# Performance work log

Hardware: AMD Instinct MI355X
Metric: run time of the kernel (lower is better)

## Reference

```python
import jax, jax.numpy as jnp
import numpy as np
import math

# Model dims (from VisionMamba defaults)
D = 768        # embed_dim
DI = 1536      # d_inner = 2*D
N = 16         # d_state
R = 48         # dt_rank = ceil(D/16)
K = 4          # d_conv
DEPTH = 24
B = 4
H, W, P, CIN = 1280, 960, 64, 3
GH, GW = H // P, W // P
NPATCH = GH * GW           # 300
L = NPATCH + 1             # 301 with cls token
POS = NPATCH // 2          # middle cls token position = 150
NCLS = 1000
EPS = 1e-5


def setup_inputs() -> dict:
    key = jax.random.key(0)
    c = [0]
    def nk():
        c[0] += 1
        return jax.random.fold_in(key, c[0])
    def rn(shape, s=0.02):
        return jax.random.normal(nk(), shape, jnp.float32) * s
    inp = {}
    inp['img'] = jax.random.normal(nk(), (B, CIN, H, W), jnp.float32)
    inp['patch_w'] = rn((D, CIN, P, P))
    inp['patch_b'] = jnp.zeros((D,), jnp.float32)
    inp['cls_token'] = rn((1, 1, D))
    inp['pos_embed'] = rn((1, L, D))
    inp['norm_w'] = jnp.ones((DEPTH, D), jnp.float32)
    inp['in_proj_w'] = rn((DEPTH, 2 * DI, D))
    for s in ('f', 'b'):
        inp[f'conv_{s}_w'] = rn((DEPTH, DI, K), 0.1)
        inp[f'conv_{s}_b'] = jnp.zeros((DEPTH, DI), jnp.float32)
        inp[f'xproj_{s}_w'] = rn((DEPTH, R + 2 * N, DI))
        inp[f'dt_{s}_w'] = rn((DEPTH, DI, R), 0.1)
        dtv = jnp.exp(jax.random.uniform(nk(), (DEPTH, DI), jnp.float32,
                                         math.log(1e-3), math.log(1e-1)))
        inp[f'dt_{s}_b'] = jnp.log(jnp.expm1(dtv))  # softplus-inverse init
        inp[f'A_{s}_log'] = jnp.broadcast_to(
            jnp.log(jnp.arange(1, N + 1, dtype=jnp.float32)), (DEPTH, DI, N)) + 0.0
        inp[f'D_{s}'] = jnp.ones((DEPTH, DI), jnp.float32)
    inp['out_proj_w'] = rn((DEPTH, D, DI))
    inp['norm_f_w'] = jnp.ones((D,), jnp.float32)
    inp['head_w'] = rn((NCLS, D))
    inp['head_b'] = jnp.zeros((NCLS,), jnp.float32)
    return inp


def _rms(x, w):
    return x * jax.lax.rsqrt(jnp.mean(x * x, axis=-1, keepdims=True) + EPS) * w


def _silu(x):
    return x * jax.nn.sigmoid(x)


def _cconv(x, w, b):
    # depthwise causal conv1d, x: [B,L,DI], w: [DI,K]
    Lx = x.shape[1]
    xp = jnp.pad(x, ((0, 0), (K - 1, 0), (0, 0)))
    return sum(xp[:, k:k + Lx, :] * w[:, k] for k in range(K)) + b


def _ssm(xc, z, xproj_w, dt_w, dt_b, A_log, Dp):
    # selective scan; xc, z: [B,L,DI]
    dbl = jnp.einsum('bld,ed->ble', xc, xproj_w)        # [B,L,R+2N]
    dt_r, Bm, Cm = dbl[..., :R], dbl[..., R:R + N], dbl[..., R + N:]
    dt = jax.nn.softplus(jnp.einsum('blr,dr->bld', dt_r, dt_w) + dt_b)
    A = -jnp.exp(A_log)                                 # [DI,N]
    dA = jnp.exp(dt[..., None] * A)                     # [B,L,DI,N]
    dBu = (dt * xc)[..., None] * Bm[:, :, None, :]      # [B,L,DI,N]
    def step(h, ab):
        a, bu = ab
        h = a * h + bu
        return h, h
    h0 = jnp.zeros((dA.shape[0], DI, N), dA.dtype)
    _, hs = jax.lax.scan(step, h0, (jnp.swapaxes(dA, 0, 1), jnp.swapaxes(dBu, 0, 1)))
    y = jnp.einsum('lbdn,bln->bld', hs, Cm) + xc * Dp
    return y * _silu(z)


def _mixer(h, p):
    (in_w, cfw, cfb, xfw, dtfw, dtfb, Afl, Df,
     cbw, cbb, xbw, dtbw, dtbb, Abl, Db, ow) = p
    xz = jnp.einsum('bld,ed->ble', h, in_w)
    x, z = xz[..., :DI], xz[..., DI:]
    yf = _ssm(_silu(_cconv(x, cfw, cfb)), z, xfw, dtfw, dtfb, Afl, Df)
    xr, zr = x[:, ::-1], z[:, ::-1]
    yb = _ssm(_silu(_cconv(xr, cbw, cbb)), zr, xbw, dtbw, dtbb, Abl, Db)
    y = (yf + yb[:, ::-1]) * 0.5   # bimamba v2 with if_divide_out=True
    return jnp.einsum('ble,de->bld', y, ow)


def _forward(img, patch_w, patch_b, cls_token, pos_embed, norm_w, in_proj_w,
             conv_f_w, conv_f_b, xproj_f_w, dt_f_w, dt_f_b, A_f_log, D_f,
             conv_b_w, conv_b_b, xproj_b_w, dt_b_w, dt_b_b, A_b_log, D_b,
             out_proj_w, norm_f_w, head_w, head_b):
    Bn = img.shape[0]
    # non-overlapping conv patch embed (kernel == stride == 64)
    x = img.reshape(Bn, CIN, GH, P, GW, P)
    x = jnp.einsum('bcipjq,dcpq->bijd', x, patch_w).reshape(Bn, NPATCH, D) + patch_b
    cls = jnp.broadcast_to(cls_token, (Bn, 1, D))
    x = jnp.concatenate([x[:, :POS], cls, x[:, POS:]], axis=1) + pos_embed
    layer_params = (norm_w, in_proj_w, conv_f_w, conv_f_b, xproj_f_w, dt_f_w,
                    dt_f_b, A_f_log, D_f, conv_b_w, conv_b_b, xproj_b_w,
                    dt_b_w, dt_b_b, A_b_log, D_b, out_proj_w)
    def layer(carry, p):
        h, res = carry
        res = res + h                # fused add-norm: Add -> RMSNorm -> Mixer
        hn = _rms(res, p[0])
        h2 = _mixer(hn, p[1:])
        return (h2, res), None
    (h, res), _ = jax.lax.scan(layer, (x, jnp.zeros_like(x)), layer_params)
    out = _rms(res + h, norm_f_w)
    return jnp.einsum('bd,cd->bc', out[:, POS], head_w) + head_b


def reference(img, patch_w, patch_b, cls_token, pos_embed, norm_w, in_proj_w,
              conv_f_w, conv_f_b, xproj_f_w, dt_f_w, dt_f_b, A_f_log, D_f,
              conv_b_w, conv_b_b, xproj_b_w, dt_b_w, dt_b_b, A_b_log, D_b,
              out_proj_w, norm_f_w, head_w, head_b):
    return _forward(img, patch_w, patch_b, cls_token, pos_embed, norm_w,
                    in_proj_w, conv_f_w, conv_f_b, xproj_f_w, dt_f_w, dt_f_b,
                    A_f_log, D_f, conv_b_w, conv_b_b, xproj_b_w, dt_b_w,
                    dt_b_b, A_b_log, D_b, out_proj_w, norm_f_w, head_w, head_b)
```

## Files before the change

kernel.cpp:

```cpp
#include <hip/hip_runtime.h>
#include <hip/hip_bf16.h>
#include <math.h>

#define B_ 4
#define L_ 301
#define D_ 768
#define DI_ 1536
#define NP_ 300
#define POS_ 150
#define M_ 1204
#define NC_ 5
#define CL_ 64

typedef __bf16 bf16;
typedef __attribute__((ext_vector_type(8))) __bf16 bf16x8;
typedef __attribute__((ext_vector_type(4))) float floatx4;

__device__ __forceinline__ float siluf(float x) { return x / (1.f + __expf(-x)); }
__device__ __forceinline__ float softplusf(float x) { return x > 20.f ? x : log1pf(__expf(x)); }

__global__ __launch_bounds__(256) void gemm_mfma(
    const bf16* __restrict__ A0, const bf16* __restrict__ A1, int lda,
    const float* __restrict__ W0, const float* __restrict__ W1, int ldw,
    const float* __restrict__ bias0, const float* __restrict__ bias1,
    float* __restrict__ C0, float* __restrict__ C1,
    bf16* __restrict__ Cb0, bf16* __restrict__ Cb1, int ldc,
    int M, int Nw, int Kw, int Ksteps, int act)
{
    const int zz = blockIdx.z;
    const bf16* A = zz ? A1 : A0;
    const float* W = zz ? W1 : W0;
    const float* bias = zz ? bias1 : bias0;
    float* C = zz ? C1 : C0;
    bf16* Cb = zz ? Cb1 : Cb0;

    __shared__ bf16 As[128 * 32];
    __shared__ bf16 Ws[128 * 32];
    const int t = threadIdx.x;
    const int bm = blockIdx.y * 128;
    const int bn = blockIdx.x * 128;
    const int lane = t & 63;
    const int wid = t >> 6;
    const int wr = wid >> 1, wc = wid & 1;
    const int ar = t >> 2;
    const int ac = (t & 3) * 8;

    const bool fullNK = ((Nw & 127) == 0) && ((Kw & 31) == 0);

    floatx4 acc[4][4] = {};

    for (int ks = 0; ks < Ksteps; ks++) {
        const int k0 = ks * 32;
#pragma unroll
        for (int c2 = 0; c2 < 2; c2++) {
            int r = ar + c2 * 64;
            int gm = bm + r; if (gm >= M) gm = M - 1;
            const bf16* gp = A + (size_t)gm * lda + k0 + ac;
            __builtin_amdgcn_global_load_lds(
                (const __attribute__((address_space(1))) void*)gp,
                (__attribute__((address_space(3))) void*)(As + r * 32 + ac),
                16, 0, 0);
        }
#pragma unroll
        for (int c2 = 0; c2 < 2; c2++) {
            int r = ar + c2 * 64;
            int gn = bn + r;
            float vv[8];
            if (fullNK) {
                const floatx4* wp4 = (const floatx4*)(W + (size_t)gn * ldw + k0 + ac);
                floatx4 a4 = wp4[0], b4 = wp4[1];
#pragma unroll
                for (int e = 0; e < 4; e++) { vv[e] = a4[e]; vv[e + 4] = b4[e]; }
            } else {
                const float* wp = W + (size_t)gn * ldw + k0 + ac;
#pragma unroll
                for (int e = 0; e < 8; e++) {
                    int kk = k0 + ac + e;
                    vv[e] = (gn < Nw && kk < Kw) ? wp[e] : 0.f;
                }
            }
            bf16x8 pk;
#pragma unroll
            for (int e = 0; e < 8; e++) pk[e] = (bf16)vv[e];
            *(bf16x8*)(Ws + r * 32 + ac) = pk;
        }
        __syncthreads();
        const int ra = wr * 64 + (lane & 15);
        const int rb = wc * 64 + (lane & 15);
        const int kb = (lane >> 4) * 8;
        bf16x8 af[4], bfm[4];
#pragma unroll
        for (int i = 0; i < 4; i++)
            af[i] = *(const bf16x8*)(As + (ra + i * 16) * 32 + kb);
#pragma unroll
        for (int j = 0; j < 4; j++)
            bfm[j] = *(const bf16x8*)(Ws + (rb + j * 16) * 32 + kb);
#pragma unroll
        for (int i = 0; i < 4; i++)
#pragma unroll
            for (int j = 0; j < 4; j++)
                acc[i][j] = __builtin_amdgcn_mfma_f32_16x16x32_bf16(af[i], bfm[j], acc[i][j], 0, 0, 0);
        __syncthreads();
    }
#pragma unroll
    for (int i = 0; i < 4; i++) {
#pragma unroll
        for (int j = 0; j < 4; j++) {
            int n = bn + wc * 64 + j * 16 + (lane & 15);
            if (n >= Nw) continue;
            float bv = (act >= 1) ? bias[n] : 0.f;
#pragma unroll
            for (int r = 0; r < 4; r++) {
                int m = bm + wr * 64 + i * 16 + (lane >> 4) * 4 + r;
                if (m >= M) continue;
                float v = acc[i][j][r] + bv;
                if (act == 2) v = softplusf(v);
                C[(size_t)m * ldc + n] = v;
                if (Cb) Cb[(size_t)m * ldc + n] = (bf16)v;
            }
        }
    }
}

__global__ __launch_bounds__(256) void gemm_mfma_sk(
    const bf16* __restrict__ A0, const bf16* __restrict__ A1, int lda,
    const float* __restrict__ W0, const float* __restrict__ W1, int ldw,
    float* __restrict__ Cp, size_t chunkStride, int ldc,
    int M, int Nw, int KstepsPer, int SK)
{
    const int z = blockIdx.z;
    const int dir = z / SK;
    const int chunk = z % SK;
    const bf16* A = dir ? A1 : A0;
    const float* W = dir ? W1 : W0;
    float* C = Cp + (size_t)z * chunkStride;

    __shared__ bf16 As[128 * 32];
    __shared__ bf16 Ws[128 * 32];
    const int t = threadIdx.x;
    const int bm = blockIdx.y * 128;
    const int bn = blockIdx.x * 128;
    const int lane = t & 63;
    const int wid = t >> 6;
    const int wr = wid >> 1, wc = wid & 1;
    const int ar = t >> 2;
    const int ac = (t & 3) * 8;

    floatx4 acc[4][4] = {};

    for (int ks = 0; ks < KstepsPer; ks++) {
        const int k0 = (chunk * KstepsPer + ks) * 32;
#pragma unroll
        for (int c2 = 0; c2 < 2; c2++) {
            int r = ar + c2 * 64;
            int gm = bm + r; if (gm >= M) gm = M - 1;
            const bf16* gp = A + (size_t)gm * lda + k0 + ac;
            __builtin_amdgcn_global_load_lds(
                (const __attribute__((address_space(1))) void*)gp,
                (__attribute__((address_space(3))) void*)(As + r * 32 + ac),
                16, 0, 0);
        }
#pragma unroll
        for (int c2 = 0; c2 < 2; c2++) {
            int r = ar + c2 * 64;
            int gn = bn + r;
            bf16x8 pk;
            if (gn < Nw) {
                const floatx4* wp4 = (const floatx4*)(W + (size_t)gn * ldw + k0 + ac);
                floatx4 a4 = wp4[0], b4 = wp4[1];
#pragma unroll
                for (int e = 0; e < 4; e++) { pk[e] = (bf16)a4[e]; pk[e + 4] = (bf16)b4[e]; }
            } else {
#pragma unroll
                for (int e = 0; e < 8; e++) pk[e] = (bf16)0.f;
            }
            *(bf16x8*)(Ws + r * 32 + ac) = pk;
        }
        __syncthreads();
        const int ra = wr * 64 + (lane & 15);
        const int rb = wc * 64 + (lane & 15);
        const int kb = (lane >> 4) * 8;
        bf16x8 af[4], bfm[4];
#pragma unroll
        for (int i = 0; i < 4; i++)
            af[i] = *(const bf16x8*)(As + (ra + i * 16) * 32 + kb);
#pragma unroll
        for (int j = 0; j < 4; j++)
            bfm[j] = *(const bf16x8*)(Ws + (rb + j * 16) * 32 + kb);
#pragma unroll
        for (int i = 0; i < 4; i++)
#pragma unroll
            for (int j = 0; j < 4; j++)
                acc[i][j] = __builtin_amdgcn_mfma_f32_16x16x32_bf16(af[i], bfm[j], acc[i][j], 0, 0, 0);
        __syncthreads();
    }
#pragma unroll
    for (int i = 0; i < 4; i++) {
#pragma unroll
        for (int j = 0; j < 4; j++) {
            int n = bn + wc * 64 + j * 16 + (lane & 15);
            if (n >= Nw) continue;
#pragma unroll
            for (int r = 0; r < 4; r++) {
                int m = bm + wr * 64 + i * 16 + (lane >> 4) * 4 + r;
                if (m >= M) continue;
                C[(size_t)m * ldc + n] = acc[i][j][r];
            }
        }
    }
}

__global__ __launch_bounds__(256) void gemm_mfma_avg_sk(
    const bf16* __restrict__ Af, const bf16* __restrict__ Ab, int lda,
    const float* __restrict__ W, int ldw,
    float* __restrict__ Cp, size_t chunkStride, int ldc,
    int M, int Nw, int KstepsPer, int SK)
{
    const int chunk = blockIdx.z;
    float* C = Cp + (size_t)chunk * chunkStride;

    __shared__ bf16 As[128 * 32];
    __shared__ bf16 Ws[128 * 32];
    const int t = threadIdx.x;
    const int bm = blockIdx.y * 128;
    const int bn = blockIdx.x * 128;
    const int lane = t & 63;
    const int wid = t >> 6;
    const int wr = wid >> 1, wc = wid & 1;
    const int ar = t >> 2;
    const int ac = (t & 3) * 8;

    floatx4 acc[4][4] = {};

    for (int ks = 0; ks < KstepsPer; ks++) {
        const int k0 = (chunk * KstepsPer + ks) * 32;
#pragma unroll
        for (int c2 = 0; c2 < 2; c2++) {
            int r = ar + c2 * 64;
            int gm = bm + r; if (gm >= M) gm = M - 1;
            bf16x8 a8 = *(const bf16x8*)(Af + (size_t)gm * lda + k0 + ac);
            bf16x8 b8 = *(const bf16x8*)(Ab + (size_t)gm * lda + k0 + ac);
            bf16x8 pk;
#pragma unroll
            for (int e = 0; e < 8; e++)
                pk[e] = (bf16)(0.5f * ((float)a8[e] + (float)b8[e]));
            *(bf16x8*)(As + r * 32 + ac) = pk;
        }
#pragma unroll
        for (int c2 = 0; c2 < 2; c2++) {
            int r = ar + c2 * 64;
            int gn = bn + r;
            const floatx4* wp4 = (const floatx4*)(W + (size_t)gn * ldw + k0 + ac);
            floatx4 a4 = wp4[0], b4 = wp4[1];
            bf16x8 pk;
#pragma unroll
            for (int e = 0; e < 4; e++) { pk[e] = (bf16)a4[e]; pk[e + 4] = (bf16)b4[e]; }
            *(bf16x8*)(Ws + r * 32 + ac) = pk;
        }
        __syncthreads();
        const int ra = wr * 64 + (lane & 15);
        const int rb = wc * 64 + (lane & 15);
        const int kb = (lane >> 4) * 8;
        bf16x8 af[4], bfm[4];
#pragma unroll
        for (int i = 0; i < 4; i++)
            af[i] = *(const bf16x8*)(As + (ra + i * 16) * 32 + kb);
#pragma unroll
        for (int j = 0; j < 4; j++)
            bfm[j] = *(const bf16x8*)(Ws + (rb + j * 16) * 32 + kb);
#pragma unroll
        for (int i = 0; i < 4; i++)
#pragma unroll
            for (int j = 0; j < 4; j++)
                acc[i][j] = __builtin_amdgcn_mfma_f32_16x16x32_bf16(af[i], bfm[j], acc[i][j], 0, 0, 0);
        __syncthreads();
    }
#pragma unroll
    for (int i = 0; i < 4; i++) {
#pragma unroll
        for (int j = 0; j < 4; j++) {
            int n = bn + wc * 64 + j * 16 + (lane & 15);
            if (n >= Nw) continue;
#pragma unroll
            for (int r = 0; r < 4; r++) {
                int m = bm + wr * 64 + i * 16 + (lane >> 4) * 4 + r;
                if (m >= M) continue;
                C[(size_t)m * ldc + n] = acc[i][j][r];
            }
        }
    }
}

__global__ void reduce_sk2(const float* __restrict__ Cp, size_t chunkStride, int SK,
                           const float* __restrict__ bias0,
                           float* __restrict__ C0, float* __restrict__ C1,
                           bf16* __restrict__ Cb0, bf16* __restrict__ Cb1,
                           int total, int ldn, int act)
{
    const int dir = blockIdx.y;
    const float* P = Cp + (size_t)dir * SK * chunkStride;
    float* C = dir ? C1 : C0;
    bf16* Cb = dir ? Cb1 : Cb0;
    int idx = blockIdx.x * 256 + threadIdx.x;
    if (idx >= total) return;
    float s = 0.f;
    for (int c = 0; c < SK; c++) s += P[(size_t)c * chunkStride + idx];
    if (act >= 1) s += bias0[idx % ldn];
    if (act == 2) s = softplusf(s);
    C[idx] = s;
    if (Cb) Cb[idx] = (bf16)s;
}

__global__ __launch_bounds__(256) void gemm_patch_mfma(
    const float* __restrict__ img, const float* __restrict__ W,
    float* __restrict__ Cp)
{
    __shared__ bf16 As[128 * 32];
    __shared__ bf16 Ws[128 * 32];
    const int t = threadIdx.x;
    const int bm = blockIdx.y * 128;
    const int bn = blockIdx.x * 128;
    const int chunk = blockIdx.z;
    const int lane = t & 63;
    const int wid = t >> 6;
    const int wr = wid >> 1, wc = wid & 1;
    const int ar = t >> 2;
    const int ac = (t & 3) * 8;
    const int M = 1200, ldw = 12288, ldc = 768;
    float* C = Cp + (size_t)chunk * M * ldc;

    const float* abase[2];
#pragma unroll
    for (int c2 = 0; c2 < 2; c2++) {
        int gm = bm + ar + c2 * 64; if (gm >= M) gm = M - 1;
        int b = gm / 300, rem = gm % 300;
        int gi = rem / 15, gj = rem % 15;
        abase[c2] = img + ((size_t)(b * 3) * 1280 + gi * 64) * 960 + gj * 64;
    }

    floatx4 acc[4][4] = {};

    for (int ks = 0; ks < 48; ks++) {
        const int k0 = (chunk * 48 + ks) * 32;
        const int k = k0 + ac;
        const int q = k & 63, p = (k >> 6) & 63, c = k >> 12;
#pragma unroll
        for (int c2 = 0; c2 < 2; c2++) {
            int r = ar + c2 * 64;
            const float* ip = abase[c2] + ((size_t)c * 1280 + p) * 960 + q;
            const floatx4* ip4 = (const floatx4*)ip;
            floatx4 a4 = ip4[0], b4 = ip4[1];
            bf16x8 pk;
#pragma unroll
            for (int e = 0; e < 4; e++) { pk[e] = (bf16)a4[e]; pk[e + 4] = (bf16)b4[e]; }
            *(bf16x8*)(As + r * 32 + ac) = pk;
        }
#pragma unroll
        for (int c2 = 0; c2 < 2; c2++) {
            int r = ar + c2 * 64;
            int gn = bn + r;
            const floatx4* wp4 = (const floatx4*)(W + (size_t)gn * ldw + k);
            floatx4 a4 = wp4[0], b4 = wp4[1];
            bf16x8 pk;
#pragma unroll
            for (int e = 0; e < 4; e++) { pk[e] = (bf16)a4[e]; pk[e + 4] = (bf16)b4[e]; }
            *(bf16x8*)(Ws + r * 32 + ac) = pk;
        }
        __syncthreads();
        const int ra = wr * 64 + (lane & 15);
        const int rb = wc * 64 + (lane & 15);
        const int kb = (lane >> 4) * 8;
        bf16x8 af[4], bfm[4];
#pragma unroll
        for (int i = 0; i < 4; i++)
            af[i] = *(const bf16x8*)(As + (ra + i * 16) * 32 + kb);
#pragma unroll
        for (int j = 0; j < 4; j++)
            bfm[j] = *(const bf16x8*)(Ws + (rb + j * 16) * 32 + kb);
#pragma unroll
        for (int i = 0; i < 4; i++)
#pragma unroll
            for (int j = 0; j < 4; j++)
                acc[i][j] = __builtin_amdgcn_mfma_f32_16x16x32_bf16(af[i], bfm[j], acc[i][j], 0, 0, 0);
        __syncthreads();
    }
#pragma unroll
    for (int i = 0; i < 4; i++) {
#pragma unroll
        for (int j = 0; j < 4; j++) {
            int n = bn + wc * 64 + j * 16 + (lane & 15);
#pragma unroll
            for (int r = 0; r < 4; r++) {
                int m = bm + wr * 64 + i * 16 + (lane >> 4) * 4 + r;
                if (m >= M) continue;
                C[(size_t)m * ldc + n] = acc[i][j][r];
            }
        }
    }
}

__global__ void gemm_bt(const float* __restrict__ A, int lda,
                        const float* __restrict__ W, int ldw,
                        const float* __restrict__ bias,
                        float* __restrict__ C, int ldc,
                        int M, int N, int K, int act) {
    __shared__ float As[16][68];
// ... 116 lines not shown
    const float* bias = rev ? bb_ : bf_;
    float* out = rev ? ob : of;
    bf16* outb = rev ? obb : ofb;
    int d = idx % DI_;
    int l = (idx / DI_) % L_;
    int b = idx / (DI_ * L_);
    float acc = bias[d];
#pragma unroll
    for (int k = 0; k < 4; k++) {
        int ls = l - 3 + k;
        if (ls < 0) continue;
        int lsrc = rev ? (L_ - 1 - ls) : ls;
        acc += xz[((long)(b * L_ + lsrc)) * (2 * DI_) + d] * w[d * 4 + k];
    }
    float v = siluf(acc);
    out[idx] = v;
    outb[idx] = (bf16)v;
}

__global__ __launch_bounds__(256) void ssm_p1(
    const float* __restrict__ xcF, const float* __restrict__ dtF, const float* __restrict__ dblF,
    const float* __restrict__ xcB, const float* __restrict__ dtB, const float* __restrict__ dblB,
    const float* __restrict__ AF, const float* __restrict__ AB,
    float* __restrict__ Hend, float* __restrict__ Aprod)
{
    const int rev = blockIdx.y;
    const int c = blockIdx.z;
    const float* xc = rev ? xcB : xcF;
    const float* dt = rev ? dtB : dtF;
    const float* dbl = rev ? dblB : dblF;
    const float* Alog = rev ? AB : AF;

    const int t = threadIdx.x;
    const int n = t & 15;
    const int g = t >> 4;
    const int gb = blockIdx.x;
    const int b = gb / (DI_ / 16);
    const int d0 = (gb % (DI_ / 16)) * 16;
    const int d = d0 + g;

    __shared__ float dt_s[CL_][16];
    __shared__ float xc_s[CL_][16];
    __shared__ float bm_s[CL_][16];

    const float a = -__expf(Alog[(size_t)d * 16 + n]);
    const size_t rowbase = (size_t)b * L_;
    const int c0 = c * CL_;

    for (int i = t; i < CL_ * 16; i += 256) {
        int ll = i >> 4, dd = i & 15;
        int l = c0 + ll;
        size_t r = (rowbase + l) * DI_ + d0 + dd;
        dt_s[ll][dd] = dt[r];
        xc_s[ll][dd] = xc[r];
        bm_s[ll][dd] = dbl[(rowbase + l) * 80 + 48 + dd];
    }
    __syncthreads();

    float h = 0.f, sdt = 0.f;
#pragma unroll 4
    for (int ll = 0; ll < CL_; ll++) {
        float dtv = dt_s[ll][g];
        float xcv = xc_s[ll][g];
        float bm = bm_s[ll][n];
        h = __expf(dtv * a) * h + dtv * xcv * bm;
        sdt += dtv;
    }
    size_t o = (((size_t)rev * (NC_ - 1) + c) * 384 + gb) * 256 + t;
    Hend[o] = h;
    Aprod[o] = __expf(a * sdt);
}

__global__ __launch_bounds__(256) void ssm_p2(
    const float* __restrict__ xcF, const float* __restrict__ dtF, const float* __restrict__ dblF,
    const float* __restrict__ xcB, const float* __restrict__ dtB, const float* __restrict__ dblB,
    const float* __restrict__ xz,
    const float* __restrict__ AF, const float* __restrict__ DF,
    const float* __restrict__ AB, const float* __restrict__ DB,
    const float* __restrict__ Hend, const float* __restrict__ Aprod,
    bf16* __restrict__ yF, bf16* __restrict__ yB)
{
    const int rev = blockIdx.y;
    const int c = blockIdx.z;
    const float* xc = rev ? xcB : xcF;
    const float* dt = rev ? dtB : dtF;
    const float* dbl = rev ? dblB : dblF;
    const float* Alog = rev ? AB : AF;
    const float* Dp = rev ? DB : DF;
    bf16* yout = rev ? yB : yF;

    const int t = threadIdx.x;
    const int n = t & 15;
    const int g = t >> 4;
    const int gb = blockIdx.x;
    const int b = gb / (DI_ / 16);
    const int d0 = (gb % (DI_ / 16)) * 16;
    const int d = d0 + g;

    __shared__ float dt_s[CL_][16];
    __shared__ float xc_s[CL_][16];
    __shared__ float z_s[CL_][16];
    __shared__ float bm_s[CL_][16];
    __shared__ float cm_s[CL_][16];
    __shared__ float y_s[CL_][16];

    const float a = -__expf(Alog[(size_t)d * 16 + n]);
    const float Dv = Dp[d];
    const size_t rowbase = (size_t)b * L_;
    const int c0 = c * CL_;
    const int Tc = min(CL_, L_ - c0);

    for (int i = t; i < Tc * 16; i += 256) {
        int ll = i >> 4, dd = i & 15;
        int l = c0 + ll;
        size_t r = (rowbase + l) * DI_ + d0 + dd;
        dt_s[ll][dd] = dt[r];
        xc_s[ll][dd] = xc[r];
        int lz = rev ? (L_ - 1 - l) : l;
        z_s[ll][dd] = xz[(rowbase + lz) * (2 * DI_) + DI_ + d0 + dd];
        bm_s[ll][dd] = dbl[(rowbase + l) * 80 + 48 + dd];
        cm_s[ll][dd] = dbl[(rowbase + l) * 80 + 64 + dd];
    }

    float h = 0.f;
    for (int j = 0; j < c; j++) {
        size_t o = (((size_t)rev * (NC_ - 1) + j) * 384 + gb) * 256 + t;
        h = Aprod[o] * h + Hend[o];
    }
    __syncthreads();

#pragma unroll 4
    for (int ll = 0; ll < Tc; ll++) {
        float dtv = dt_s[ll][g];
        float xcv = xc_s[ll][g];
        float bm = bm_s[ll][n];
        float cm = cm_s[ll][n];
        h = __expf(dtv * a) * h + dtv * xcv * bm;
        float cc = h * cm;
        cc += __shfl_xor(cc, 1);
        cc += __shfl_xor(cc, 2);
        cc += __shfl_xor(cc, 4);
        cc += __shfl_xor(cc, 8);
        if (n == 0) {
            float yv = (cc + xcv * Dv) * siluf(z_s[ll][g]);
            y_s[ll][g] = yv;
        }
    }
    __syncthreads();

    for (int i = t; i < Tc * 16; i += 256) {
        int ll = i >> 4, dd = i & 15;
        int l = c0 + ll;
        int lo = rev ? (L_ - 1 - l) : l;
        yout[(rowbase + lo) * DI_ + d0 + dd] = (bf16)y_s[ll][dd];
    }
}

__global__ void final_rms(const float* __restrict__ res, const float* __restrict__ h,
                          const float* __restrict__ w, float* __restrict__ out) {
    int b = blockIdx.x;
    long base = ((long)b * L_ + POS_) * D_;
    float v[3];
    float ss = 0.f;
#pragma unroll
    for (int i = 0; i < 3; i++) {
        int d = threadIdx.x + i * 256;
        float t = res[base + d] + h[base + d];
        v[i] = t;
        ss += t * t;
    }
#pragma unroll
    for (int off = 1; off < 64; off <<= 1) ss += __shfl_xor(ss, off);
    __shared__ float red[4];
    __shared__ float inv;
    if ((threadIdx.x & 63) == 0) red[threadIdx.x >> 6] = ss;
    __syncthreads();
    if (threadIdx.x == 0) {
// ... 37 lines not shown
    const float* norm_f_w = (const float*)d_in[22];
    const float* head_w = (const float*)d_in[23];
    const float* head_b = (const float*)d_in[24];

    char* p8 = (char*)d_ws;
    auto alloc = [&](size_t nb) { char* r = p8; p8 += (nb + 255) & ~(size_t)255; return r; };
    float* x    = (float*)alloc((size_t)M_ * D_ * 4);
    float* res  = (float*)alloc((size_t)M_ * D_ * 4);
    bf16*  hnb  = (bf16*) alloc((size_t)M_ * D_ * 2);
    float* xz   = (float*)alloc((size_t)M_ * 2 * DI_ * 4);
    float* xcf  = (float*)alloc((size_t)M_ * DI_ * 4);
    float* xcb  = (float*)alloc((size_t)M_ * DI_ * 4);
    bf16*  xcfb = (bf16*) alloc((size_t)M_ * DI_ * 2);
    bf16*  xcbb = (bf16*) alloc((size_t)M_ * DI_ * 2);
    float* dtf  = (float*)alloc((size_t)M_ * DI_ * 4);
    float* dtb  = (float*)alloc((size_t)M_ * DI_ * 4);
    bf16*  yfb  = (bf16*) alloc((size_t)M_ * DI_ * 2);
    bf16*  ybb  = (bf16*) alloc((size_t)M_ * DI_ * 2);
    float* dblf = (float*)alloc((size_t)M_ * 80 * 4);
    float* dblb = (float*)alloc((size_t)M_ * 80 * 4);
    bf16*  dblfb= (bf16*) alloc((size_t)M_ * 80 * 2);
    bf16*  dblbb= (bf16*) alloc((size_t)M_ * 80 * 2);
    float* clsv = (float*)alloc((size_t)B_ * D_ * 4);
    float* hend = (float*)alloc((size_t)2 * (NC_ - 1) * 384 * 256 * 4);
    float* aprd = (float*)alloc((size_t)2 * (NC_ - 1) * 384 * 256 * 4);
    float* xtmp = dtf;

    float* patchP = xz;
    float* xprojP = dtf;
    float* outP   = dtf;

    gemm_patch_mfma<<<dim3(6, 10, 8), 256, 0, stream>>>(img, patch_w, patchP);
    reduce_sk2<<<dim3((1200 * 768 + 255) / 256, 1), 256, 0, stream>>>(
        patchP, (size_t)1200 * 768, 8, patch_b, xtmp, nullptr, nullptr, nullptr,
        1200 * 768, 768, 1);
    assemble<<<(B_ * L_ * D_ + 255) / 256, 256, 0, stream>>>(xtmp, cls_token, pos_embed, x, res);

    for (int layer = 0; layer < 24; layer++) {
        const float* ipw = in_proj_w + (size_t)layer * 2 * DI_ * D_;
        const float* cfw = conv_f_w + (size_t)layer * DI_ * 4;
        const float* cfb = conv_f_b + (size_t)layer * DI_;
        const float* xfw = xproj_f_w + (size_t)layer * 80 * DI_;
        const float* dfw = dt_f_w + (size_t)layer * DI_ * 48;
        const float* dfb = dt_f_b + (size_t)layer * DI_;
        const float* afl = A_f_log + (size_t)layer * DI_ * 16;
        const float* df = D_f + (size_t)layer * DI_;
        const float* cbw = conv_b_w + (size_t)layer * DI_ * 4;
        const float* cbb = conv_b_b + (size_t)layer * DI_;
        const float* xbw = xproj_b_w + (size_t)layer * 80 * DI_;
        const float* dbw = dt_b_w + (size_t)layer * DI_ * 48;
        const float* dbb = dt_b_b + (size_t)layer * DI_;
        const float* abl = A_b_log + (size_t)layer * DI_ * 16;
        const float* db = D_b + (size_t)layer * DI_;
        const float* opw = out_proj_w + (size_t)layer * D_ * DI_;
        const float* nw = norm_w + (size_t)layer * D_;

        add_rms<<<M_, 256, 0, stream>>>(res, x, nw, hnb);
        gemm_mfma<<<dim3(24, 10, 1), 256, 0, stream>>>(
            hnb, hnb, D_, ipw, ipw, D_, nullptr, nullptr,
            xz, xz, nullptr, nullptr, 2 * DI_, M_, 2 * DI_, D_, 24, 0);
        conv_silu2<<<dim3((B_ * L_ * DI_ + 255) / 256, 2), 256, 0, stream>>>(
            xz, cfw, cfb, cbw, cbb, xcf, xcfb, xcb, xcbb);
        gemm_mfma_sk<<<dim3(1, 10, 16), 256, 0, stream>>>(
            xcfb, xcbb, DI_, xfw, xbw, DI_,
            xprojP, (size_t)M_ * 80, 80, M_, 80, 6, 8);
        reduce_sk2<<<dim3((M_ * 80 + 255) / 256, 2), 256, 0, stream>>>(
            xprojP, (size_t)M_ * 80, 8, nullptr,
            dblf, dblb, dblfb, dblbb, M_ * 80, 80, 0);
        gemm_mfma<<<dim3(12, 10, 2), 256, 0, stream>>>(
            dblfb, dblbb, 80, dfw, dbw, 48, dfb, dbb,
            dtf, dtb, nullptr, nullptr, DI_, M_, DI_, 48, 2, 2);
        ssm_p1<<<dim3(384, 2, NC_ - 1), 256, 0, stream>>>(
            xcf, dtf, dblf, xcb, dtb, dblb, afl, abl, hend, aprd);
        ssm_p2<<<dim3(384, 2, NC_), 256, 0, stream>>>(
            xcf, dtf, dblf, xcb, dtb, dblb, xz, afl, df, abl, db,
            hend, aprd, yfb, ybb);
        gemm_mfma_avg_sk<<<dim3(6, 10, 4), 256, 0, stream>>>(
            yfb, ybb, DI_, opw, DI_,
            outP, (size_t)M_ * D_, D_, M_, D_, 12, 4);
        reduce_sk2<<<dim3((M_ * D_ + 255) / 256, 1), 256, 0, stream>>>(
            outP, (size_t)M_ * D_, 4, nullptr,
            x, nullptr, nullptr, nullptr, M_ * D_, D_, 0);
    }

    final_rms<<<B_, 256, 0, stream>>>(res, x, norm_f_w, clsv);
    gemm_bt<<<dim3(16, 1), 256, 0, stream>>>(clsv, D_, head_w, D_, head_b,
                                             (float*)d_out, 1000, B_, 1000, D_, 1);
}
```

Measured before the change: 6.487 ms.

## Double-buffer LDS tiles in all GEMMs and restructure SSM scan per channel

```diff
diff --git a/kernel.cpp b/kernel.cpp
--- a/kernel.cpp
+++ b/kernel.cpp
@@ -34,8 +34,8 @@
     float* C = zz ? C1 : C0;
     bf16* Cb = zz ? Cb1 : Cb0;
 
-    __shared__ bf16 As[128 * 32];
-    __shared__ bf16 Ws[128 * 32];
+    __shared__ bf16 As[2][128 * 32];
+    __shared__ bf16 Ws[2][128 * 32];
     const int t = threadIdx.x;
     const int bm = blockIdx.y * 128;
     const int bn = blockIdx.x * 128;
@@ -44,62 +44,106 @@
     const int wr = wid >> 1, wc = wid & 1;
     const int ar = t >> 2;
     const int ac = (t & 3) * 8;
-
     const bool fullNK = ((Nw & 127) == 0) && ((Kw & 31) == 0);
 
+    int gmr[2], gnr[2];
+#pragma unroll
+    for (int c2 = 0; c2 < 2; c2++) {
+        int gm = bm + ar + c2 * 64; if (gm >= M) gm = M - 1;
+        gmr[c2] = gm;
+        gnr[c2] = bn + ar + c2 * 64;
+    }
+
     floatx4 acc[4][4] = {};
+    float vv[2][8];
+
+#pragma unroll
+    for (int c2 = 0; c2 < 2; c2++) {
+        const bf16* gp = A + (size_t)gmr[c2] * lda + ac;
+        __builtin_amdgcn_global_load_lds(
+            (const __attribute__((address_space(1))) void*)gp,
+            (__attribute__((address_space(3))) void*)(&As[0][0] + (ar + c2 * 64) * 32 + ac),
+            16, 0, 0);
+    }
+#pragma unroll
+    for (int c2 = 0; c2 < 2; c2++) {
+        if (fullNK) {
+            const floatx4* wp4 = (const floatx4*)(W + (size_t)gnr[c2] * ldw + ac);
+            floatx4 a4 = wp4[0], b4 = wp4[1];
+#pragma unroll
+            for (int e = 0; e < 4; e++) { vv[c2][e] = a4[e]; vv[c2][e + 4] = b4[e]; }
+        } else {
+            const float* wp = W + (size_t)gnr[c2] * ldw + ac;
+#pragma unroll
+            for (int e = 0; e < 8; e++) {
+                int kk = ac + e;
+                vv[c2][e] = (gnr[c2] < Nw && kk < Kw) ? wp[e] : 0.f;
+            }
+        }
+    }
+#pragma unroll
+    for (int c2 = 0; c2 < 2; c2++) {
+        bf16x8 pk;
+#pragma unroll
+        for (int e = 0; e < 8; e++) pk[e] = (bf16)vv[c2][e];
+        *(bf16x8*)(&Ws[0][0] + (ar + c2 * 64) * 32 + ac) = pk;
+    }
+    __syncthreads();
 
     for (int ks = 0; ks < Ksteps; ks++) {
-        const int k0 = ks * 32;
-#pragma unroll
-        for (int c2 = 0; c2 < 2; c2++) {
-            int r = ar + c2 * 64;
-            int gm = bm + r; if (gm >= M) gm = M - 1;
-            const bf16* gp = A + (size_t)gm * lda + k0 + ac;
-            __builtin_amdgcn_global_load_lds(
-                (const __attribute__((address_space(1))) void*)gp,
-                (__attribute__((address_space(3))) void*)(As + r * 32 + ac),
-                16, 0, 0);
-        }
-#pragma unroll
-        for (int c2 = 0; c2 < 2; c2++) {
-            int r = ar + c2 * 64;
-            int gn = bn + r;
-            float vv[8];
-            if (fullNK) {
-                const floatx4* wp4 = (const floatx4*)(W + (size_t)gn * ldw + k0 + ac);
-                floatx4 a4 = wp4[0], b4 = wp4[1];
-#pragma unroll
-                for (int e = 0; e < 4; e++) { vv[e] = a4[e]; vv[e + 4] = b4[e]; }
-            } else {
-                const float* wp = W + (size_t)gn * ldw + k0 + ac;
-#pragma unroll
-                for (int e = 0; e < 8; e++) {
-                    int kk = k0 + ac + e;
-                    vv[e] = (gn < Nw && kk < Kw) ? wp[e] : 0.f;
+        const int cur = ks & 1, nxt = cur ^ 1;
+        const bool pf = (ks + 1 < Ksteps);
+        if (pf) {
+            const int k0 = (ks + 1) * 32;
+#pragma unroll
+            for (int c2 = 0; c2 < 2; c2++) {
+                const bf16* gp = A + (size_t)gmr[c2] * lda + k0 + ac;
+                __builtin_amdgcn_global_load_lds(
+                    (const __attribute__((address_space(1))) void*)gp,
+                    (__attribute__((address_space(3))) void*)(&As[nxt][0] + (ar + c2 * 64) * 32 + ac),
+                    16, 0, 0);
+            }
+#pragma unroll
+            for (int c2 = 0; c2 < 2; c2++) {
+                if (fullNK) {
+                    const floatx4* wp4 = (const floatx4*)(W + (size_t)gnr[c2] * ldw + k0 + ac);
+                    floatx4 a4 = wp4[0], b4 = wp4[1];
+#pragma unroll
+                    for (int e = 0; e < 4; e++) { vv[c2][e] = a4[e]; vv[c2][e + 4] = b4[e]; }
+                } else {
+                    const float* wp = W + (size_t)gnr[c2] * ldw + k0 + ac;
+#pragma unroll
+                    for (int e = 0; e < 8; e++) {
+                        int kk = k0 + ac + e;
+                        vv[c2][e] = (gnr[c2] < Nw && kk < Kw) ? wp[e] : 0.f;
+                    }
                 }
             }
-            bf16x8 pk;
-#pragma unroll
-            for (int e = 0; e < 8; e++) pk[e] = (bf16)vv[e];
-            *(bf16x8*)(Ws + r * 32 + ac) = pk;
-        }
-        __syncthreads();
+        }
         const int ra = wr * 64 + (lane & 15);
         const int rb = wc * 64 + (lane & 15);
         const int kb = (lane >> 4) * 8;
         bf16x8 af[4], bfm[4];
 #pragma unroll
         for (int i = 0; i < 4; i++)
-            af[i] = *(const bf16x8*)(As + (ra + i * 16) * 32 + kb);
+            af[i] = *(const bf16x8*)(&As[cur][0] + (ra + i * 16) * 32 + kb);
 #pragma unroll
         for (int j = 0; j < 4; j++)
-            bfm[j] = *(const bf16x8*)(Ws + (rb + j * 16) * 32 + kb);
+            bfm[j] = *(const bf16x8*)(&Ws[cur][0] + (rb + j * 16) * 32 + kb);
 #pragma unroll
         for (int i = 0; i < 4; i++)
 #pragma unroll
             for (int j = 0; j < 4; j++)
                 acc[i][j] = __builtin_amdgcn_mfma_f32_16x16x32_bf16(af[i], bfm[j], acc[i][j], 0, 0, 0);
+        if (pf) {
+#pragma unroll
+            for (int c2 = 0; c2 < 2; c2++) {
+                bf16x8 pk;
+#pragma unroll
+                for (int e = 0; e < 8; e++) pk[e] = (bf16)vv[c2][e];
+                *(bf16x8*)(&Ws[nxt][0] + (ar + c2 * 64) * 32 + ac) = pk;
+            }
+        }
         __syncthreads();
     }
 #pragma unroll
@@ -134,9 +178,10 @@
     const bf16* A = dir ? A1 : A0;
     const float* W = dir ? W1 : W0;
     float* C = Cp + (size_t)z * chunkStride;
-
-    __shared__ bf16 As[128 * 32];
-    __shared__ bf16 Ws[128 * 32];
+    const int kbase = chunk * KstepsPer * 32;
+
+    __shared__ bf16 As[2][128 * 32];
+    __shared__ bf16 Ws[2][128 * 32];
     const int t = threadIdx.x;
     const int bm = blockIdx.y * 128;
     const int bn = blockIdx.x * 128;
@@ -146,52 +191,96 @@
     const int ar = t >> 2;
     const int ac = (t & 3) * 8;
 
+    int gmr[2], gnr[2];
+#pragma unroll
+    for (int c2 = 0; c2 < 2; c2++) {
+        int gm = bm + ar + c2 * 64; if (gm >= M) gm = M - 1;
+        gmr[c2] = gm;
+        gnr[c2] = bn + ar + c2 * 64;
+    }
+
     floatx4 acc[4][4] = {};
+    float vv[2][8];
+
+#pragma unroll
+    for (int c2 = 0; c2 < 2; c2++) {
+        const bf16* gp = A + (size_t)gmr[c2] * lda + kbase + ac;
+        __builtin_amdgcn_global_load_lds(
+            (const __attribute__((address_space(1))) void*)gp,
+            (__attribute__((address_space(3))) void*)(&As[0][0] + (ar + c2 * 64) * 32 + ac),
+            16, 0, 0);
+    }
+#pragma unroll
+    for (int c2 = 0; c2 < 2; c2++) {
+        if (gnr[c2] < Nw) {
+            const floatx4* wp4 = (const floatx4*)(W + (size_t)gnr[c2] * ldw + kbase + ac);
+            floatx4 a4 = wp4[0], b4 = wp4[1];
+#pragma unroll
+            for (int e = 0; e < 4; e++) { vv[c2][e] = a4[e]; vv[c2][e + 4] = b4[e]; }
+        } else {
+#pragma unroll
+            for (int e = 0; e < 8; e++) vv[c2][e] = 0.f;
+        }
+    }
+#pragma unroll
+    for (int c2 = 0; c2 < 2; c2++) {
+        bf16x8 pk;
+#pragma unroll
+        for (int e = 0; e < 8; e++) pk[e] = (bf16)vv[c2][e];
+        *(bf16x8*)(&Ws[0][0] + (ar + c2 * 64) * 32 + ac) = pk;
+    }
+    __syncthreads();
 
     for (int ks = 0; ks < KstepsPer; ks++) {
-        const int k0 = (chunk * KstepsPer + ks) * 32;
-#pragma unroll
-        for (int c2 = 0; c2 < 2; c2++) {
-            int r = ar + c2 * 64;
-            int gm = bm + r; if (gm >= M) gm = M - 1;
-            const bf16* gp = A + (size_t)gm * lda + k0 + ac;
-            __builtin_amdgcn_global_load_lds(
-                (const __attribute__((address_space(1))) void*)gp,
-                (__attribute__((address_space(3))) void*)(As + r * 32 + ac),
-                16, 0, 0);
-        }
-#pragma unroll
-        for (int c2 = 0; c2 < 2; c2++) {
-            int r = ar + c2 * 64;
-            int gn = bn + r;
-            bf16x8 pk;
-            if (gn < Nw) {
-                const floatx4* wp4 = (const floatx4*)(W + (size_t)gn * ldw + k0 + ac);
-                floatx4 a4 = wp4[0], b4 = wp4[1];
-#pragma unroll
-                for (int e = 0; e < 4; e++) { pk[e] = (bf16)a4[e]; pk[e + 4] = (bf16)b4[e]; }
-            } else {
-#pragma unroll
-                for (int e = 0; e < 8; e++) pk[e] = (bf16)0.f;
-            }
-            *(bf16x8*)(Ws + r * 32 + ac) = pk;
-        }
-        __syncthreads();
+        const int cur = ks & 1, nxt = cur ^ 1;
+        const bool pf = (ks + 1 < KstepsPer);
+        if (pf) {
+            const int k0 = kbase + (ks + 1) * 32;
+#pragma unroll
+            for (int c2 = 0; c2 < 2; c2++) {
+                const bf16* gp = A + (size_t)gmr[c2] * lda + k0 + ac;
+                __builtin_amdgcn_global_load_lds(
+                    (const __attribute__((address_space(1))) void*)gp,
+                    (__attribute__((address_space(3))) void*)(&As[nxt][0] + (ar + c2 * 64) * 32 + ac),
+                    16, 0, 0);
+            }
+#pragma unroll
+            for (int c2 = 0; c2 < 2; c2++) {
+                if (gnr[c2] < Nw) {
+                    const floatx4* wp4 = (const floatx4*)(W + (size_t)gnr[c2] * ldw + k0 + ac);
+                    floatx4 a4 = wp4[0], b4 = wp4[1];
+#pragma unroll
+                    for (int e = 0; e < 4; e++) { vv[c2][e] = a4[e]; vv[c2][e + 4] = b4[e]; }
+                } else {
+#pragma unroll
+                    for (int e = 0; e < 8; e++) vv[c2][e] = 0.f;
+                }
+            }
+        }
         const int ra = wr * 64 + (lane & 15);
         const int rb = wc * 64 + (lane & 15);
         const int kb = (lane >> 4) * 8;
         bf16x8 af[4], bfm[4];
 #pragma unroll
         for (int i = 0; i < 4; i++)
-            af[i] = *(const bf16x8*)(As + (ra + i * 16) * 32 + kb);
+            af[i] = *(const bf16x8*)(&As[cur][0] + (ra + i * 16) * 32 + kb);
 #pragma unroll
         for (int j = 0; j < 4; j++)
-            bfm[j] = *(const bf16x8*)(Ws + (rb + j * 16) * 32 + kb);
+            bfm[j] = *(const bf16x8*)(&Ws[cur][0] + (rb + j * 16) * 32 + kb);
 #pragma unroll
         for (int i = 0; i < 4; i++)
 #pragma unroll
             for (int j = 0; j < 4; j++)
                 acc[i][j] = __builtin_amdgcn_mfma_f32_16x16x32_bf16(af[i], bfm[j], acc[i][j], 0, 0, 0);
+        if (pf) {
+#pragma unroll
+            for (int c2 = 0; c2 < 2; c2++) {
+                bf16x8 pk;
+#pragma unroll
+                for (int e = 0; e < 8; e++) pk[e] = (bf16)vv[c2][e];
+                *(bf16x8*)(&Ws[nxt][0] + (ar + c2 * 64) * 32 + ac) = pk;
+            }
+        }
         __syncthreads();
     }
 #pragma unroll
@@ -218,9 +307,10 @@
 {
     const int chunk = blockIdx.z;
     float* C = Cp + (size_t)chunk * chunkStride;
-
-    __shared__ bf16 As[128 * 32];
-    __shared__ bf16 Ws[128 * 32];
+    const int kbase = chunk * KstepsPer * 32;
+
+    __shared__ bf16 As[2][128 * 32];
+    __shared__ bf16 Ws[2][128 * 32];
     const int t = threadIdx.x;
     const int bm = blockIdx.y * 128;
     const int bn = blockIdx.x * 128;
@@ -230,49 +320,83 @@
     const int ar = t >> 2;
     const int ac = (t & 3) * 8;
 
+    int gmr[2], gnr[2];
+#pragma unroll
+    for (int c2 = 0; c2 < 2; c2++) {
+        int gm = bm + ar + c2 * 64; if (gm >= M) gm = M - 1;
+        gmr[c2] = gm;
+        gnr[c2] = bn + ar + c2 * 64;
+    }
+
     floatx4 acc[4][4] = {};
+    bf16x8 a8[2], b8[2];
+    float vv[2][8];
+
+#pragma unroll
+    for (int c2 = 0; c2 < 2; c2++) {
+        a8[c2] = *(const bf16x8*)(Af + (size_t)gmr[c2] * lda + kbase + ac);
+        b8[c2] = *(const bf16x8*)(Ab + (size_t)gmr[c2] * lda + kbase + ac);
+        const floatx4* wp4 = (const floatx4*)(W + (size_t)gnr[c2] * ldw + kbase + ac);
+        floatx4 w4 = wp4[0], x4 = wp4[1];
+#pragma unroll
+        for (int e = 0; e < 4; e++) { vv[c2][e] = w4[e]; vv[c2][e + 4] = x4[e]; }
+    }
+#pragma unroll
+    for (int c2 = 0; c2 < 2; c2++) {
+        bf16x8 pa, pw;
+#pragma unroll
+        for (int e = 0; e < 8; e++) {
+            pa[e] = (bf16)(0.5f * ((float)a8[c2][e] + (float)b8[c2][e]));
+            pw[e] = (bf16)vv[c2][e];
+        }
+        *(bf16x8*)(&As[0][0] + (ar + c2 * 64) * 32 + ac) = pa;
+        *(bf16x8*)(&Ws[0][0] + (ar + c2 * 64) * 32 + ac) = pw;
+    }
+    __syncthreads();
 
     for (int ks = 0; ks < KstepsPer; ks++) {
-        const int k0 = (chunk * KstepsPer + ks) * 32;
-#pragma unroll
-        for (int c2 = 0; c2 < 2; c2++) {
-            int r = ar + c2 * 64;
-            int gm = bm + r; if (gm >= M) gm = M - 1;
-            bf16x8 a8 = *(const bf16x8*)(Af + (size_t)gm * lda + k0 + ac);
-            bf16x8 b8 = *(const bf16x8*)(Ab + (size_t)gm * lda + k0 + ac);
-            bf16x8 pk;
-#pragma unroll
-            for (int e = 0; e < 8; e++)
-                pk[e] = (bf16)(0.5f * ((float)a8[e] + (float)b8[e]));
-            *(bf16x8*)(As + r * 32 + ac) = pk;
-        }
-#pragma unroll
-        for (int c2 = 0; c2 < 2; c2++) {
-            int r = ar + c2 * 64;
-            int gn = bn + r;
-            const floatx4* wp4 = (const floatx4*)(W + (size_t)gn * ldw + k0 + ac);
-            floatx4 a4 = wp4[0], b4 = wp4[1];
-            bf16x8 pk;
-#pragma unroll
-            for (int e = 0; e < 4; e++) { pk[e] = (bf16)a4[e]; pk[e + 4] = (bf16)b4[e]; }
-            *(bf16x8*)(Ws + r * 32 + ac) = pk;
-        }
-        __syncthreads();
+        const int cur = ks & 1, nxt = cur ^ 1;
+        const bool pf = (ks + 1 < KstepsPer);
+        if (pf) {
+            const int k0 = kbase + (ks + 1) * 32;
+#pragma unroll
+            for (int c2 = 0; c2 < 2; c2++) {
+                a8[c2] = *(const bf16x8*)(Af + (size_t)gmr[c2] * lda + k0 + ac);
+                b8[c2] = *(const bf16x8*)(Ab + (size_t)gmr[c2] * lda + k0 + ac);
+                const floatx4* wp4 = (const floatx4*)(W + (size_t)gnr[c2] * ldw + k0 + ac);
+                floatx4 w4 = wp4[0], x4 = wp4[1];
+#pragma unroll
+                for (int e = 0; e < 4; e++) { vv[c2][e] = w4[e]; vv[c2][e + 4] = x4[e]; }
+            }
+        }
         const int ra = wr * 64 + (lane & 15);
         const int rb = wc * 64 + (lane & 15);
         const int kb = (lane >> 4) * 8;
         bf16x8 af[4], bfm[4];
 #pragma unroll
         for (int i = 0; i < 4; i++)
-            af[i] = *(const bf16x8*)(As + (ra + i * 16) * 32 + kb);
+            af[i] = *(const bf16x8*)(&As[cur][0] + (ra + i * 16) * 32 + kb);
 #pragma unroll
         for (int j = 0; j < 4; j++)
-            bfm[j] = *(const bf16x8*)(Ws + (rb + j * 16) * 32 + kb);
+            bfm[j] = *(const bf16x8*)(&Ws[cur][0] + (rb + j * 16) * 32 + kb);
 #pragma unroll
         for (int i = 0; i < 4; i++)
 #pragma unroll
             for (int j = 0; j < 4; j++)
                 acc[i][j] = __builtin_amdgcn_mfma_f32_16x16x32_bf16(af[i], bfm[j], acc[i][j], 0, 0, 0);
+        if (pf) {
+#pragma unroll
+            for (int c2 = 0; c2 < 2; c2++) {
+                bf16x8 pa, pw;
+#pragma unroll
+                for (int e = 0; e < 8; e++) {
+                    pa[e] = (bf16)(0.5f * ((float)a8[c2][e] + (float)b8[c2][e]));
+                    pw[e] = (bf16)vv[c2][e];
+                }
+                *(bf16x8*)(&As[nxt][0] + (ar + c2 * 64) * 32 + ac) = pa;
+                *(bf16x8*)(&Ws[nxt][0] + (ar + c2 * 64) * 32 + ac) = pw;
+            }
+        }
         __syncthreads();
     }
 #pragma unroll
@@ -315,8 +439,8 @@
     const float* __restrict__ img, const float* __restrict__ W,
     float* __restrict__ Cp)
 {
-    __shared__ bf16 As[128 * 32];
-    __shared__ bf16 Ws[128 * 32];
+    __shared__ bf16 As[2][128 * 32];
+    __shared__ bf16 Ws[2][128 * 32];
     const int t = threadIdx.x;
     const int bm = blockIdx.y * 128;
     const int bn = blockIdx.x * 128;
@@ -327,61 +451,93 @@
     const int ar = t >> 2;
     const int ac = (t & 3) * 8;
     const int M = 1200, ldw = 12288, ldc = 768;
+    const int kbase = chunk * 1536;
     float* C = Cp + (size_t)chunk * M * ldc;
 
     const float* abase[2];
+    int gnr[2];
 #pragma unroll
     for (int c2 = 0; c2 < 2; c2++) {
         int gm = bm + ar + c2 * 64; if (gm >= M) gm = M - 1;
         int b = gm / 300, rem = gm % 300;
         int gi = rem / 15, gj = rem % 15;
         abase[c2] = img + ((size_t)(b * 3) * 1280 + gi * 64) * 960 + gj * 64;
+        gnr[c2] = bn + ar + c2 * 64;
     }
 
     floatx4 acc[4][4] = {};
+    float av[2][8], vv[2][8];
+
+    {
+        const int k = kbase + ac;
+        const int q = k & 63, p = (k >> 6) & 63, c = k >> 12;
+#pragma unroll
+        for (int c2 = 0; c2 < 2; c2++) {
+            const floatx4* ip4 = (const floatx4*)(abase[c2] + ((size_t)c * 1280 + p) * 960 + q);
+            floatx4 i4 = ip4[0], j4 = ip4[1];
+            const floatx4* wp4 = (const floatx4*)(W + (size_t)gnr[c2] * ldw + k);
+            floatx4 w4 = wp4[0], x4 = wp4[1];
+#pragma unroll
+            for (int e = 0; e < 4; e++) {
+                av[c2][e] = i4[e]; av[c2][e + 4] = j4[e];
+                vv[c2][e] = w4[e]; vv[c2][e + 4] = x4[e];
+            }
+        }
+#pragma unroll
+        for (int c2 = 0; c2 < 2; c2++) {
+            bf16x8 pa, pw;
+#pragma unroll
+            for (int e = 0; e < 8; e++) { pa[e] = (bf16)av[c2][e]; pw[e] = (bf16)vv[c2][e]; }
+            *(bf16x8*)(&As[0][0] + (ar + c2 * 64) * 32 + ac) = pa;
+            *(bf16x8*)(&Ws[0][0] + (ar + c2 * 64) * 32 + ac) = pw;
+        }
+    }
+    __syncthreads();
 
     for (int ks = 0; ks < 48; ks++) {
-        const int k0 = (chunk * 48 + ks) * 32;
-        const int k = k0 + ac;
-        const int q = k & 63, p = (k >> 6) & 63, c = k >> 12;
-#pragma unroll
-        for (int c2 = 0; c2 < 2; c2++) {
-            int r = ar + c2 * 64;
-            const float* ip = abase[c2] + ((size_t)c * 1280 + p) * 960 + q;
-            const floatx4* ip4 = (const floatx4*)ip;
-            floatx4 a4 = ip4[0], b4 = ip4[1];
-            bf16x8 pk;
-#pragma unroll
-            for (int e = 0; e < 4; e++) { pk[e] = (bf16)a4[e]; pk[e + 4] = (bf16)b4[e]; }
-            *(bf16x8*)(As + r * 32 + ac) = pk;
-        }
-#pragma unroll
-        for (int c2 = 0; c2 < 2; c2++) {
-            int r = ar + c2 * 64;
-            int gn = bn + r;
-            const floatx4* wp4 = (const floatx4*)(W + (size_t)gn * ldw + k);
-            floatx4 a4 = wp4[0], b4 = wp4[1];
-            bf16x8 pk;
-#pragma unroll
-            for (int e = 0; e < 4; e++) { pk[e] = (bf16)a4[e]; pk[e + 4] = (bf16)b4[e]; }
-            *(bf16x8*)(Ws + r * 32 + ac) = pk;
-        }
-        __syncthreads();
+        const int cur = ks & 1, nxt = cur ^ 1;
+        const bool pf = (ks + 1 < 48);
+        if (pf) {
+            const int k = kbase + (ks + 1) * 32 + ac;
+            const int q = k & 63, p = (k >> 6) & 63, c = k >> 12;
+#pragma unroll
+            for (int c2 = 0; c2 < 2; c2++) {
+                const floatx4* ip4 = (const floatx4*)(abase[c2] + ((size_t)c * 1280 + p) * 960 + q);
+                floatx4 i4 = ip4[0], j4 = ip4[1];
+                const floatx4* wp4 = (const floatx4*)(W + (size_t)gnr[c2] * ldw + k);
+                floatx4 w4 = wp4[0], x4 = wp4[1];
+#pragma unroll
+                for (int e = 0; e < 4; e++) {
+                    av[c2][e] = i4[e]; av[c2][e + 4] = j4[e];
+                    vv[c2][e] = w4[e]; vv[c2][e + 4] = x4[e];
+                }
+            }
+        }
         const int ra = wr * 64 + (lane & 15);
         const int rb = wc * 64 + (lane & 15);
         const int kb = (lane >> 4) * 8;
         bf16x8 af[4], bfm[4];
 #pragma unroll
         for (int i = 0; i < 4; i++)
-            af[i] = *(const bf16x8*)(As + (ra + i * 16) * 32 + kb);
+            af[i] = *(const bf16x8*)(&As[cur][0] + (ra + i * 16) * 32 + kb);
 #pragma unroll
         for (int j = 0; j < 4; j++)
-            bfm[j] = *(const bf16x8*)(Ws + (rb + j * 16) * 32 + kb);
+            bfm[j] = *(const bf16x8*)(&Ws[cur][0] + (rb + j * 16) * 32 + kb);
 #pragma unroll
         for (int i = 0; i < 4; i++)
 #pragma unroll
             for (int j = 0; j < 4; j++)
                 acc[i][j] = __builtin_amdgcn_mfma_f32_16x16x32_bf16(af[i], bfm[j], acc[i][j], 0, 0, 0);
+        if (pf) {
+#pragma unroll
+            for (int c2 = 0; c2 < 2; c2++) {
+                bf16x8 pa, pw;
+#pragma unroll
+                for (int e = 0; e < 8; e++) { pa[e] = (bf16)av[c2][e]; pw[e] = (bf16)vv[c2][e]; }
+                *(bf16x8*)(&As[nxt][0] + (ar + c2 * 64) * 32 + ac) = pa;
+                *(bf16x8*)(&Ws[nxt][0] + (ar + c2 * 64) * 32 + ac) = pw;
+            }
+        }
         __syncthreads();
     }
 #pragma unroll
@@ -544,7 +700,7 @@
     const float* __restrict__ xcF, const float* __restrict__ dtF, const float* __restrict__ dblF,
     const float* __restrict__ xcB, const float* __restrict__ dtB, const float* __restrict__ dblB,
     const float* __restrict__ AF, const float* __restrict__ AB,
-    float* __restrict__ Hend, float* __restrict__ Aprod)
+    float* __restrict__ Hend, float* __restrict__ Sdt)
 {
     const int rev = blockIdx.y;
     const int c = blockIdx.z;
@@ -554,43 +710,48 @@
     const float* Alog = rev ? AB : AF;
 
     const int t = threadIdx.x;
-    const int n = t & 15;
-    const int g = t >> 4;
     const int gb = blockIdx.x;
-    const int b = gb / (DI_ / 16);
-    const int d0 = (gb % (DI_ / 16)) * 16;
-    const int d = d0 + g;
-
-    __shared__ float dt_s[CL_][16];
-    __shared__ float xc_s[CL_][16];
+    const int b = gb / (DI_ / 256);
+    const int d = (gb % (DI_ / 256)) * 256 + t;
+
     __shared__ float bm_s[CL_][16];
-
-    const float a = -__expf(Alog[(size_t)d * 16 + n]);
     const size_t rowbase = (size_t)b * L_;
     const int c0 = c * CL_;
 
     for (int i = t; i < CL_ * 16; i += 256) {
-        int ll = i >> 4, dd = i & 15;
-        int l = c0 + ll;
-        size_t r = (rowbase + l) * DI_ + d0 + dd;
-        dt_s[ll][dd] = dt[r];
-        xc_s[ll][dd] = xc[r];
-        bm_s[ll][dd] = dbl[(rowbase + l) * 80 + 48 + dd];
+        int ll = i >> 4, n = i & 15;
+        bm_s[ll][n] = dbl[(rowbase + c0 + ll) * 80 + 48 + n];
+    }
+
+    float a[16];
+    const floatx4* ap = (const floatx4*)(Alog + (size_t)d * 16);
+#pragma unroll
+    for (int q = 0; q < 4; q++) {
+        floatx4 v = ap[q];
+#pragma unroll
+        for (int e = 0; e < 4; e++) a[q * 4 + e] = -__expf(v[e]);
     }
     __syncthreads();
 
-    float h = 0.f, sdt = 0.f;
-#pragma unroll 4
+    float h[16];
+#pragma unroll
+    for (int n = 0; n < 16; n++) h[n] = 0.f;
+    float sdt = 0.f;
     for (int ll = 0; ll < CL_; ll++) {
-        float dtv = dt_s[ll][g];
-        float xcv = xc_s[ll][g];
-        float bm = bm_s[ll][n];
-        h = __expf(dtv * a) * h + dtv * xcv * bm;
+        size_t r = (rowbase + c0 + ll) * DI_ + d;
+        float dtv = dt[r];
+        float xcv = xc[r];
+        float dbu = dtv * xcv;
         sdt += dtv;
-    }
-    size_t o = (((size_t)rev * (NC_ - 1) + c) * 384 + gb) * 256 + t;
-    Hend[o] = h;
-    Aprod[o] = __expf(a * sdt);
+#pragma unroll
+        for (int n = 0; n < 16; n++)
+            h[n] = __expf(dtv * a[n]) * h[n] + dbu * bm_s[ll][n];
+    }
+    size_t ob = (size_t)(rev * (NC_ - 1) + c) * B_ + b;
+#pragma unroll
+    for (int n = 0; n < 16; n++)
+        Hend[(ob * 16 + n) * DI_ + d] = h[n];
+    Sdt[ob * DI_ + d] = sdt;
 }
 
 __global__ __launch_bounds__(256) void ssm_p2(
@@ -599,7 +760,7 @@
     const float* __restrict__ xz,
     const float* __restrict__ AF, const float* __restrict__ DF,
     const float* __restrict__ AB, const float* __restrict__ DB,
-    const float* __restrict__ Hend, const float* __restrict__ Aprod,
+    const float* __restrict__ Hend, const float* __restrict__ Sdt,
     bf16* __restrict__ yF, bf16* __restrict__ yB)
 {
     const int rev = blockIdx.y;
@@ -612,69 +773,61 @@
     bf16* yout = rev ? yB : yF;
 
     const int t = threadIdx.x;
-    const int n = t & 15;
-    const int g = t >> 4;
     const int gb = blockIdx.x;
-    const int b = gb / (DI_ / 16);
-    const int d0 = (gb % (DI_ / 16)) * 16;
-    const int d = d0 + g;
-
-    __shared__ float dt_s[CL_][16];
-    __shared__ float xc_s[CL_][16];
-    __shared__ float z_s[CL_][16];
+    const int b = gb / (DI_ / 256);
+    const int d = (gb % (DI_ / 256)) * 256 + t;
+
     __shared__ float bm_s[CL_][16];
     __shared__ float cm_s[CL_][16];
-    __shared__ float y_s[CL_][16];
-
-    const float a = -__expf(Alog[(size_t)d * 16 + n]);
-    const float Dv = Dp[d];
     const size_t rowbase = (size_t)b * L_;
     const int c0 = c * CL_;
     const int Tc = min(CL_, L_ - c0);
 
     for (int i = t; i < Tc * 16; i += 256) {
-        int ll = i >> 4, dd = i & 15;
+        int ll = i >> 4, n = i & 15;
+        size_t rb8 = (rowbase + c0 + ll) * 80;
+        bm_s[ll][n] = dbl[rb8 + 48 + n];
+        cm_s[ll][n] = dbl[rb8 + 64 + n];
+    }
+
+    float a[16];
+    const floatx4* ap = (const floatx4*)(Alog + (size_t)d * 16);
+#pragma unroll
+    for (int q = 0; q < 4; q++) {
+        floatx4 v = ap[q];
+#pragma unroll
+        for (int e = 0; e < 4; e++) a[q * 4 + e] = -__expf(v[e]);
+    }
+    const float Dv = Dp[d];
+
+    float h[16];
+#pragma unroll
+    for (int n = 0; n < 16; n++) h[n] = 0.f;
+    for (int j = 0; j < c; j++) {
+        size_t ob = (size_t)(rev * (NC_ - 1) + j) * B_ + b;
+        float sd = Sdt[ob * DI_ + d];
+#pragma unroll
+        for (int n = 0; n < 16; n++)
+            h[n] = __expf(a[n] * sd) * h[n] + Hend[(ob * 16 + n) * DI_ + d];
+    }
+    __syncthreads();
+
+    for (int ll = 0; ll < Tc; ll++) {
         int l = c0 + ll;
-        size_t r = (rowbase + l) * DI_ + d0 + dd;
-        dt_s[ll][dd] = dt[r];
-        xc_s[ll][dd] = xc[r];
-        int lz = rev ? (L_ - 1 - l) : l;
-        z_s[ll][dd] = xz[(rowbase + lz) * (2 * DI_) + DI_ + d0 + dd];
-        bm_s[ll][dd] = dbl[(rowbase + l) * 80 + 48 + dd];
-        cm_s[ll][dd] = dbl[(rowbase + l) * 80 + 64 + dd];
-    }
-
-    float h = 0.f;
-    for (int j = 0; j < c; j++) {
-        size_t o = (((size_t)rev * (NC_ - 1) + j) * 384 + gb) * 256 + t;
-        h = Aprod[o] * h + Hend[o];
-    }
-    __syncthreads();
-
-#pragma unroll 4
-    for (int ll = 0; ll < Tc; ll++) {
-        float dtv = dt_s[ll][g];
-        float xcv = xc_s[ll][g];
-        float bm = bm_s[ll][n];
-        float cm = cm_s[ll][n];
-        h = __expf(dtv * a) * h + dtv * xcv * bm;
-        float cc = h * cm;
-        cc += __shfl_xor(cc, 1);
-        cc += __shfl_xor(cc, 2);
-        cc += __shfl_xor(cc, 4);
-        cc += __shfl_xor(cc, 8);
-        if (n == 0) {
-            float yv = (cc + xcv * Dv) * siluf(z_s[ll][g]);
-            y_s[ll][g] = yv;
-        }
-    }
-    __syncthreads();
-
-    for (int i = t; i < Tc * 16; i += 256) {
-        int ll = i >> 4, dd = i & 15;
-        int l = c0 + ll;
+        size_t r = (rowbase + l) * DI_ + d;
+        float dtv = dt[r];
+        float xcv = xc[r];
         int lo = rev ? (L_ - 1 - l) : l;
-        yout[(rowbase + lo) * DI_ + d0 + dd] = (bf16)y_s[ll][dd];
+        float zv = xz[(rowbase + lo) * (2 * DI_) + DI_ + d];
+        float dbu = dtv * xcv;
+        float acc2 = 0.f;
+#pragma unroll
+        for (int n = 0; n < 16; n++) {
+            h[n] = __expf(dtv * a[n]) * h[n] + dbu * bm_s[ll][n];
+            acc2 += h[n] * cm_s[ll][n];
+        }
+        float yv = (acc2 + xcv * Dv) * siluf(zv);
+        yout[(rowbase + lo) * DI_ + d] = (bf16)yv;
     }
 }
 
@@ -758,8 +911,8 @@
     bf16*  dblfb= (bf16*) alloc((size_t)M_ * 80 * 2);
     bf16*  dblbb= (bf16*) alloc((size_t)M_ * 80 * 2);
     float* clsv = (float*)alloc((size_t)B_ * D_ * 4);
-    float* hend = (float*)alloc((size_t)2 * (NC_ - 1) * 384 * 256 * 4);
-    float* aprd = (float*)alloc((size_t)2 * (NC_ - 1) * 384 * 256 * 4);
+    float* hend = (float*)alloc((size_t)2 * (NC_ - 1) * B_ * 16 * DI_ * 4);
+    float* sdtb = (float*)alloc((size_t)2 * (NC_ - 1) * B_ * DI_ * 4);
     float* xtmp = dtf;
 
     float* patchP = xz;
@@ -806,11 +959,11 @@
         gemm_mfma<<<dim3(12, 10, 2), 256, 0, stream>>>(
             dblfb, dblbb, 80, dfw, dbw, 48, dfb, dbb,
             dtf, dtb, nullptr, nullptr, DI_, M_, DI_, 48, 2, 2);
-        ssm_p1<<<dim3(384, 2, NC_ - 1), 256, 0, stream>>>(
-            xcf, dtf, dblf, xcb, dtb, dblb, afl, abl, hend, aprd);
-        ssm_p2<<<dim3(384, 2, NC_), 256, 0, stream>>>(
+        ssm_p1<<<dim3(24, 2, NC_ - 1), 256, 0, stream>>>(
+            xcf, dtf, dblf, xcb, dtb, dblb, afl, abl, hend, sdtb);
+        ssm_p2<<<dim3(24, 2, NC_), 256, 0, stream>>>(
             xcf, dtf, dblf, xcb, dtb, dblb, xz, afl, df, abl, db,
-            hend, aprd, yfb, ybb);
+            hend, sdtb, yfb, ybb);
         gemm_mfma_avg_sk<<<dim3(6, 10, 4), 256, 0, stream>>>(
             yfb, ybb, DI_, opw, DI_,
             outP, (size_t)M_ * D_, D_, M_, D_, 12, 4);
```

Result: faster. 5.968 ms (-8.0%).
